# Performance work log

Hardware: AMD Instinct MI355X
Metric: run time of the kernel (lower is better)

The kernel has to match this reference:

```python
import jax, jax.numpy as jnp
import numpy as np


def reference(x, weight, bias):
    """Per-sample dynamic conv2d, expressed as one grouped convolution.

    x:      (B, C_in, H, W)
    weight: (B, C_out, C_in, kH, kW)
    bias:   (B, C_out)
    returns (B, C_out, H_out, W_out) with H_out = H - kH + 1 (valid conv)
    """
    B, C_in, H, W = x.shape
    C_out, kH, kW = weight.shape[1], weight.shape[3], weight.shape[4]
    # Fold batch into channels: groups=B grouped conv == B independent convs.
    x_g = x.reshape(1, B * C_in, H, W)
    w_g = weight.reshape(B * C_out, C_in, kH, kW)
    out = jax.lax.conv_general_dilated(
        x_g, w_g,
        window_strides=(1, 1),
        padding='VALID',
        dimension_numbers=('NCHW', 'OIHW', 'NCHW'),
        feature_group_count=B,
    )  # (1, B*C_out, H_out, W_out)
    out = out.reshape(B, C_out, out.shape[2], out.shape[3])
    return out + bias[:, :, None, None]


def setup_inputs() -> dict:
    key = jax.random.key(0)
    k1, k2, k3 = jax.random.split(key, 3)
    B, C_in, C_out, H, W, kH, kW = 16, 64, 64, 128, 128, 3, 3
    x = jax.random.normal(k1, (B, C_in, H, W), dtype=jnp.float32)
    weight = jax.random.normal(k2, (B, C_out, C_in, kH, kW), dtype=jnp.float32) * 0.05
    bias = jax.random.normal(k3, (B, C_out), dtype=jnp.float32)
    return {"x": x, "weight": weight, "bias": bias}
```

## Files before the change

### kernel.cpp

```cpp
#include <hip/hip_runtime.h>
#include <hip/hip_bf16.h>

#define BATCH 16
#define CI 64
#define CO 64
#define H 128
#define W 128
#define HO 126
#define WO 126
#define HW (H * W)

typedef short bfrag __attribute__((ext_vector_type(8)));
typedef float ffrag __attribute__((ext_vector_type(4)));

typedef __attribute__((address_space(1))) const unsigned char g_byte;
typedef __attribute__((address_space(3))) unsigned char l_byte;

static __device__ __forceinline__ unsigned short f2bf(float f) {
    unsigned u = __float_as_uint(f);
    u += 0x7fffu + ((u >> 16) & 1u);
    return (unsigned short)(u >> 16);
}

__global__ void wt_prepass(const float* __restrict__ w, unsigned short* __restrict__ w_t) {
    int i = blockIdx.x * 256 + threadIdx.x;
    int ci = i & 63;
    int co = (i >> 6) & 63;
    int bs = i >> 12;
    int b = bs / 9, s = bs - b * 9;
    w_t[i] = f2bf(w[(((b * 64 + co) * 64 + ci) * 9) + s]);
}

__global__ void xt_prepass(const float* __restrict__ x, unsigned short* __restrict__ x_t) {
    __shared__ __align__(16) float lf[64 * 132];
    const int row = blockIdx.x, b = blockIdx.y, t = threadIdx.x;

    const float* xb = x + (size_t)b * CI * HW + (size_t)row * W;
    {
        const int ci0 = t >> 5, c4 = (t & 31) * 4;
        #pragma unroll
        for (int p = 0; p < 8; ++p) {
            const int ci = p * 8 + ci0;
            float4 v = *(const float4*)(xb + (size_t)ci * HW + c4);
            *(float4*)&lf[ci * 132 + c4] = v;
        }
    }
    __syncthreads();
    unsigned short* xrow = x_t + ((size_t)(b * 128) + row) * 8192;
    #pragma unroll
    for (int cc = 0; cc < 4; ++cc) {
        const int c = cc * 256 + t;
        const int col = c >> 3, s8 = c & 7, o = s8 ^ (col & 7);
        unsigned int u[4];
        #pragma unroll
        for (int e = 0; e < 4; ++e) {
            float f0 = lf[(o * 8 + 2 * e) * 132 + col];
            float f1 = lf[(o * 8 + 2 * e + 1) * 132 + col];
            __hip_bfloat162 h2 = __float22bfloat162_rn(make_float2(f0, f1));
            u[e] = *(unsigned int*)&h2;
        }
        *(uint4*)&xrow[(size_t)c * 8] = *(const uint4*)u;
    }
}

__launch_bounds__(256)
__global__ void dynconv_fused(const unsigned short* __restrict__ x_t,
                              const unsigned short* __restrict__ w_t,
                              const float* __restrict__ bias,
                              float* __restrict__ out) {
    __shared__ __align__(16) unsigned short xs[5 * 8192];

    const int tid = threadIdx.x;
    const int gx  = blockIdx.x;
    const int b   = blockIdx.y;
    const int y0  = gx * 4;
    const int nu  = (gx == 31) ? 2 : 4;
    const int rmaxl = nu + 1;

    const int wave = tid >> 6, lane = tid & 63;
    const int l16 = lane & 15, lq = lane >> 4;

    const bfrag* wtb = (const bfrag*)w_t + (size_t)(b * 9) * 512;
    const int co_b = wave * 16 + l16;
    bfrag a[9][2];
    #pragma unroll
    for (int s = 0; s < 9; ++s)
        #pragma unroll
        for (int ks = 0; ks < 2; ++ks)
            a[s][ks] = wtb[s * 512 + co_b * 8 + ks * 4 + lq];

    float bv[4];
    #pragma unroll
    for (int r = 0; r < 4; ++r)
        bv[r] = bias[b * 64 + wave * 16 + lq * 4 + r];

    const unsigned short* xtb = x_t + ((size_t)(b * 128) + y0) * 8192;
    const int lnoff = wave * 4096 + lane * 16;

#define STAGE_ROW(RL, SL)                                                       \
    do {                                                                        \
        const char* gsrc_ = (const char*)(xtb + (size_t)(RL) * 8192) + lnoff;   \
        l_byte* ldst_ = (l_byte*)((char*)&xs[(SL) * 8192] + wave * 4096);       \
        _Pragma("unroll") for (int q_ = 0; q_ < 4; ++q_)                        \
            __builtin_amdgcn_global_load_lds((g_byte*)(gsrc_ + q_ * 1024),      \
                                             ldst_ + q_ * 1024, 16, 0, 0);      \
    } while (0)

    #pragma unroll
    for (int r = 0; r < 5; ++r) {
        const int rl = (r <= rmaxl) ? r : rmaxl;
        STAGE_ROW(rl, r);
    }
    asm volatile("s_waitcnt vmcnt(8)" ::: "memory");
    __builtin_amdgcn_s_barrier();
    __builtin_amdgcn_sched_barrier(0);

    for (int j = 0; j < nu; ++j) {
        ffrag acc[8];
        #pragma unroll
        for (int nt = 0; nt < 8; ++nt) acc[nt] = (ffrag){0.f, 0.f, 0.f, 0.f};

        #pragma unroll
        for (int s = 0; s < 9; ++s) {
            const int dy = s / 3, dx = s - dy * 3;
            int t = j + dy; if (t >= 5) t -= 5;
            const unsigned short* slabp = &xs[t * 8192];
            #pragma unroll
            for (int ks = 0; ks < 2; ++ks) {
                const int o = ks * 4 + lq;
                #pragma unroll
                for (int nt = 0; nt < 8; ++nt) {
                    int colx = nt * 16 + l16 + dx;
                    if (colx > 127) colx = 127;
                    const bfrag bf = *(const bfrag*)&slabp[(colx * 8 + (o ^ (colx & 7))) * 8];
                    acc[nt] = __builtin_amdgcn_mfma_f32_16x16x32_bf16(a[s][ks], bf, acc[nt], 0, 0, 0);
                }
            }
        }

        asm volatile("s_waitcnt lgkmcnt(0)" ::: "memory");
        __builtin_amdgcn_s_barrier();
        __builtin_amdgcn_sched_barrier(0);

        {
            const int rl = (j + 5 <= rmaxl) ? (j + 5) : rmaxl;
            STAGE_ROW(rl, j);
        }
        __builtin_amdgcn_sched_barrier(0);

        if (j == 0) { asm volatile("s_waitcnt vmcnt(8)"  ::: "memory"); }
        else        { asm volatile("s_waitcnt vmcnt(36)" ::: "memory"); }
        __builtin_amdgcn_s_barrier();
        __builtin_amdgcn_sched_barrier(0);

        const int oy = y0 + j;
        #pragma unroll
        for (int r = 0; r < 4; ++r) {
            float* op = out + ((size_t)(b * 64 + wave * 16 + lq * 4 + r) * HO + oy) * WO;
            const float bvv = bv[r];
            #pragma unroll
            for (int nt = 0; nt < 8; ++nt) {
                const int ox = nt * 16 + l16;
                if (ox < WO) op[ox] = acc[nt][r] + bvv;
            }
        }
    }
#undef STAGE_ROW
}

extern "C" void kernel_launch(void* const* d_in, const int* in_sizes, int n_in,
                              void* d_out, int out_size, void* d_ws, size_t ws_size,
                              hipStream_t stream) {
    const float* x    = (const float*)d_in[0];
    const float* w    = (const float*)d_in[1];
    const float* bias = (const float*)d_in[2];
    float* out        = (float*)d_out;

    unsigned short* w_t = (unsigned short*)d_ws;
    unsigned short* x_t = (unsigned short*)((char*)d_ws + 1179648);

    wt_prepass<<<dim3(589824 / 256), dim3(256), 0, stream>>>(w, w_t);
    xt_prepass<<<dim3(128, BATCH), dim3(256), 0, stream>>>(x, x_t);
    dynconv_fused<<<dim3(32, BATCH), dim3(256), 0, stream>>>(x_t, w_t, bias, out);
}
```

Measured before the change: 146.9 us.

## Fuse prepass kernels and split conv columns across eight waves per block

The weight and input transpose/bf16 prepasses are merged into one kernel launch, with each block also converting a 288-element slice of the weights. The main conv kernel moves to 512 threads. Each wave now covers 16 output channels over one 64-column half, so it holds 4 accumulators instead of 8. The LDS row ring shrinks from 5 slots to 4, with the vmcnt wait counts updated to match. The aim is more waves in flight to hide latency and one fewer launch, at the cost of less B-fragment reuse per wave and a shallower prefetch ring.

```diff
diff --git a/kernel.cpp b/kernel.cpp
--- a/kernel.cpp
+++ b/kernel.cpp
@@ -22,18 +22,26 @@
     return (unsigned short)(u >> 16);
 }
 
-__global__ void wt_prepass(const float* __restrict__ w, unsigned short* __restrict__ w_t) {
-    int i = blockIdx.x * 256 + threadIdx.x;
-    int ci = i & 63;
-    int co = (i >> 6) & 63;
-    int bs = i >> 12;
-    int b = bs / 9, s = bs - b * 9;
-    w_t[i] = f2bf(w[(((b * 64 + co) * 64 + ci) * 9) + s]);
-}
-
-__global__ void xt_prepass(const float* __restrict__ x, unsigned short* __restrict__ x_t) {
+__global__ void prepass(const float* __restrict__ x, const float* __restrict__ w,
+                        unsigned short* __restrict__ x_t, unsigned short* __restrict__ w_t) {
     __shared__ __align__(16) float lf[64 * 132];
     const int row = blockIdx.x, b = blockIdx.y, t = threadIdx.x;
+
+    {
+        const int base = (b * 128 + row) * 288;
+        int i = base + t;
+        {
+            int ci = i & 63, co = (i >> 6) & 63, bs = i >> 12;
+            int bw = bs / 9, s = bs - bw * 9;
+            w_t[i] = f2bf(w[(((bw * 64 + co) * 64 + ci) * 9) + s]);
+        }
+        if (t < 32) {
+            i = base + 256 + t;
+            int ci = i & 63, co = (i >> 6) & 63, bs = i >> 12;
+            int bw = bs / 9, s = bs - bw * 9;
+            w_t[i] = f2bf(w[(((bw * 64 + co) * 64 + ci) * 9) + s]);
+        }
+    }
 
     const float* xb = x + (size_t)b * CI * HW + (size_t)row * W;
     {
@@ -41,8 +49,7 @@
         #pragma unroll
         for (int p = 0; p < 8; ++p) {
             const int ci = p * 8 + ci0;
-            float4 v = *(const float4*)(xb + (size_t)ci * HW + c4);
-            *(float4*)&lf[ci * 132 + c4] = v;
+            *(float4*)&lf[ci * 132 + c4] = *(const float4*)(xb + (size_t)ci * HW + c4);
         }
     }
     __syncthreads();
@@ -54,21 +61,20 @@
         unsigned int u[4];
         #pragma unroll
         for (int e = 0; e < 4; ++e) {
-            float f0 = lf[(o * 8 + 2 * e) * 132 + col];
-            float f1 = lf[(o * 8 + 2 * e + 1) * 132 + col];
-            __hip_bfloat162 h2 = __float22bfloat162_rn(make_float2(f0, f1));
+            __hip_bfloat162 h2 = __float22bfloat162_rn(make_float2(
+                lf[(o * 8 + 2 * e) * 132 + col], lf[(o * 8 + 2 * e + 1) * 132 + col]));
             u[e] = *(unsigned int*)&h2;
         }
         *(uint4*)&xrow[(size_t)c * 8] = *(const uint4*)u;
     }
 }
 
-__launch_bounds__(256)
+__launch_bounds__(512)
 __global__ void dynconv_fused(const unsigned short* __restrict__ x_t,
                               const unsigned short* __restrict__ w_t,
                               const float* __restrict__ bias,
                               float* __restrict__ out) {
-    __shared__ __align__(16) unsigned short xs[5 * 8192];
+    __shared__ __align__(16) unsigned short xs[4 * 8192];
 
     const int tid = threadIdx.x;
     const int gx  = blockIdx.x;
@@ -79,9 +85,11 @@
 
     const int wave = tid >> 6, lane = tid & 63;
     const int l16 = lane & 15, lq = lane >> 4;
+    const int wq = wave & 3;
+    const int wc = wave >> 2;
 
     const bfrag* wtb = (const bfrag*)w_t + (size_t)(b * 9) * 512;
-    const int co_b = wave * 16 + l16;
+    const int co_b = wq * 16 + l16;
     bfrag a[9][2];
     #pragma unroll
     for (int s = 0; s < 9; ++s)
@@ -89,48 +97,44 @@
         for (int ks = 0; ks < 2; ++ks)
             a[s][ks] = wtb[s * 512 + co_b * 8 + ks * 4 + lq];
 
-    float bv[4];
-    #pragma unroll
-    for (int r = 0; r < 4; ++r)
-        bv[r] = bias[b * 64 + wave * 16 + lq * 4 + r];
+    const float4 bvv4 = *(const float4*)&bias[b * 64 + wq * 16 + lq * 4];
 
     const unsigned short* xtb = x_t + ((size_t)(b * 128) + y0) * 8192;
-    const int lnoff = wave * 4096 + lane * 16;
+    const int lnoff = tid * 16;
 
 #define STAGE_ROW(RL, SL)                                                       \
     do {                                                                        \
-        const char* gsrc_ = (const char*)(xtb + (size_t)(RL) * 8192) + lnoff;   \
-        l_byte* ldst_ = (l_byte*)((char*)&xs[(SL) * 8192] + wave * 4096);       \
-        _Pragma("unroll") for (int q_ = 0; q_ < 4; ++q_)                        \
-            __builtin_amdgcn_global_load_lds((g_byte*)(gsrc_ + q_ * 1024),      \
-                                             ldst_ + q_ * 1024, 16, 0, 0);      \
+        const char* gsrc_ = (const char*)(xtb + (size_t)(RL) * 8192);           \
+        _Pragma("unroll") for (int q_ = 0; q_ < 2; ++q_)                        \
+            __builtin_amdgcn_global_load_lds(                                   \
+                (g_byte*)(gsrc_ + lnoff + q_ * 8192),                           \
+                (l_byte*)((char*)&xs[(SL) * 8192] + wave * 1024 + q_ * 8192),   \
+                16, 0, 0);                                                      \
     } while (0)
 
+    __builtin_amdgcn_sched_barrier(0);
+
     #pragma unroll
-    for (int r = 0; r < 5; ++r) {
-        const int rl = (r <= rmaxl) ? r : rmaxl;
-        STAGE_ROW(rl, r);
-    }
-    asm volatile("s_waitcnt vmcnt(8)" ::: "memory");
+    for (int r = 0; r < 4; ++r) STAGE_ROW(r, r);
+    asm volatile("s_waitcnt vmcnt(2)" ::: "memory");
     __builtin_amdgcn_s_barrier();
     __builtin_amdgcn_sched_barrier(0);
 
     for (int j = 0; j < nu; ++j) {
-        ffrag acc[8];
+        ffrag acc[4];
         #pragma unroll
-        for (int nt = 0; nt < 8; ++nt) acc[nt] = (ffrag){0.f, 0.f, 0.f, 0.f};
+        for (int nt = 0; nt < 4; ++nt) acc[nt] = (ffrag){0.f, 0.f, 0.f, 0.f};
 
         #pragma unroll
         for (int s = 0; s < 9; ++s) {
             const int dy = s / 3, dx = s - dy * 3;
-            int t = j + dy; if (t >= 5) t -= 5;
-            const unsigned short* slabp = &xs[t * 8192];
+            const unsigned short* slabp = &xs[((j + dy) & 3) * 8192];
             #pragma unroll
             for (int ks = 0; ks < 2; ++ks) {
                 const int o = ks * 4 + lq;
                 #pragma unroll
-                for (int nt = 0; nt < 8; ++nt) {
-                    int colx = nt * 16 + l16 + dx;
+                for (int nt = 0; nt < 4; ++nt) {
+                    int colx = wc * 64 + nt * 16 + l16 + dx;
                     if (colx > 127) colx = 127;
                     const bfrag bf = *(const bfrag*)&slabp[(colx * 8 + (o ^ (colx & 7))) * 8];
                     acc[nt] = __builtin_amdgcn_mfma_f32_16x16x32_bf16(a[s][ks], bf, acc[nt], 0, 0, 0);
@@ -143,24 +147,24 @@
         __builtin_amdgcn_sched_barrier(0);
 
         {
-            const int rl = (j + 5 <= rmaxl) ? (j + 5) : rmaxl;
-            STAGE_ROW(rl, j);
+            const int rl = (j + 4 <= rmaxl) ? (j + 4) : rmaxl;
+            STAGE_ROW(rl, j & 3);
         }
         __builtin_amdgcn_sched_barrier(0);
 
-        if (j == 0) { asm volatile("s_waitcnt vmcnt(8)"  ::: "memory"); }
-        else        { asm volatile("s_waitcnt vmcnt(36)" ::: "memory"); }
+        if (j == 0) { asm volatile("s_waitcnt vmcnt(2)"  ::: "memory"); }
+        else        { asm volatile("s_waitcnt vmcnt(18)" ::: "memory"); }
         __builtin_amdgcn_s_barrier();
         __builtin_amdgcn_sched_barrier(0);
 
         const int oy = y0 + j;
         #pragma unroll
         for (int r = 0; r < 4; ++r) {
-            float* op = out + ((size_t)(b * 64 + wave * 16 + lq * 4 + r) * HO + oy) * WO;
-            const float bvv = bv[r];
+            float* op = out + ((size_t)(b * 64 + wq * 16 + lq * 4 + r) * HO + oy) * WO;
+            const float bvv = ((const float*)&bvv4)[r];
             #pragma unroll
-            for (int nt = 0; nt < 8; ++nt) {
-                const int ox = nt * 16 + l16;
+            for (int nt = 0; nt < 4; ++nt) {
+                const int ox = wc * 64 + nt * 16 + l16;
                 if (ox < WO) op[ox] = acc[nt][r] + bvv;
             }
         }
@@ -179,7 +183,6 @@
     unsigned short* w_t = (unsigned short*)d_ws;
     unsigned short* x_t = (unsigned short*)((char*)d_ws + 1179648);
 
-    wt_prepass<<<dim3(589824 / 256), dim3(256), 0, stream>>>(w, w_t);
-    xt_prepass<<<dim3(128, BATCH), dim3(256), 0, stream>>>(x, x_t);
-    dynconv_fused<<<dim3(32, BATCH), dim3(256), 0, stream>>>(x_t, w_t, bias, out);
+    prepass<<<dim3(128, BATCH), dim3(256), 0, stream>>>(x, w, x_t, w_t);
+    dynconv_fused<<<dim3(32, BATCH), dim3(512), 0, stream>>>(x_t, w_t, bias, out);
 }
```

New measurement: 149.2 us. Within noise of the previous version (+1.6%).
